# Kernel optimization log

Hardware: AMD Instinct MI355X
Metric: run time of the kernel (lower is better)

The kernel has to match this reference:

```python
import jax, jax.numpy as jnp
import numpy as np

B, N, H, D, HID = 4, 1024, 16, 72, 1152
ATT = H * D

def setup_inputs() -> dict:
    key = jax.random.key(0)
    ks = jax.random.split(key, 5)
    s = 0.02
    return {
        "x": jax.random.normal(ks[0], (B, N, HID), dtype=jnp.float32),
        "w_qkv": jax.random.normal(ks[1], (HID, 3 * ATT), dtype=jnp.float32) * s,
        "b_qkv": jnp.zeros((3 * ATT,), dtype=jnp.float32),
        "w_out": jax.random.normal(ks[2], (ATT, HID), dtype=jnp.float32) * s,
        "b_out": jnp.zeros((HID,), dtype=jnp.float32),
    }

def reference(x, w_qkv, b_qkv, w_out, b_out):
    # QKV projection: [B,N,3*ATT]
    qkv = x @ w_qkv + b_qkv
    q, k, v = jnp.split(qkv, 3, axis=-1)
    # [B,N,H,D] -> [B,H,N,D]
    q = q.reshape(B, N, H, D).transpose(0, 2, 1, 3)
    k = k.reshape(B, N, H, D).transpose(0, 2, 1, 3)
    v = v.reshape(B, N, H, D).transpose(0, 2, 1, 3)
    scale = D ** -0.5
    att = jnp.einsum("bhqd,bhkd->bhqk", q, k) * scale
    att = jax.nn.softmax(att, axis=-1)
    out = jnp.einsum("bhqk,bhkd->bhqd", att, v)
    out = out.transpose(0, 2, 1, 3).reshape(B, N, ATT)
    return out @ w_out + b_out
```

## Files before the change

kernel.cpp:

```cpp
#include <hip/hip_runtime.h>
#include <cstdint>

#define NB 4
#define NSEQ 1024
#define NH 16
#define HD 72
#define HID 1152
#define QKV3 3456
#define DP 96
#define QSCALE 0.17003713711193175f

typedef __attribute__((ext_vector_type(8))) __bf16 bf16x8;
typedef __attribute__((ext_vector_type(4))) __bf16 bf16x4;
typedef __attribute__((ext_vector_type(4))) float f32x4;

#define AS1 __attribute__((address_space(1)))
#define AS3 __attribute__((address_space(3)))

__device__ __forceinline__ void gl_lds16(const void* g, void* l) {
    __builtin_amdgcn_global_load_lds((const AS1 uint32_t*)g, (AS3 uint32_t*)l, 16, 0, 0);
}

#define RAW_BAR() asm volatile("s_barrier" ::: "memory")

__device__ __forceinline__ float fast_exp2(float x) {
    float r;
    asm("v_exp_f32 %0, %1" : "=v"(r) : "v"(x));
    return r;
}

#define XB_OFF     0UL
#define WQKVT_OFF  9437184UL
#define WOUTT_OFF  17694720UL
#define QP_OFF     20643840UL
#define KP_OFF     33226752UL
#define VT_OFF     45809664UL


__global__ void prep_kernel(const float* __restrict__ x, __bf16* __restrict__ xb,
                            const float* __restrict__ w_qkv, __bf16* __restrict__ wqkvT,
                            const float* __restrict__ w_out, __bf16* __restrict__ woutT,
                            __bf16* __restrict__ Qp, __bf16* __restrict__ Kp,
                            __bf16* __restrict__ Vt) {
    __shared__ float t[32][33];
    const int blk = blockIdx.x, tid = threadIdx.x;
    if (blk < 4608) {
        long i = (long)blk * 256 + tid;
        float4 v = ((const float4*)x)[i];
        bf16x4 o = { (__bf16)v.x, (__bf16)v.y, (__bf16)v.z, (__bf16)v.w };
        ((bf16x4*)xb)[i] = o;
    } else if (blk < 9792) {
        const float* in;  __bf16* outp;  int Nc, K, n0, k0;
        if (blk < 8496) {
            int b = blk - 4608; in = w_qkv; outp = wqkvT; Nc = QKV3; K = HID;
            n0 = (b % 108) * 32; k0 = (b / 108) * 32;
        } else {
            int b = blk - 8496; in = w_out; outp = woutT; Nc = HID; K = HID;
            n0 = (b % 36) * 32; k0 = (b / 36) * 32;
        }
        int xx = tid & 31, yy = tid >> 5;
        #pragma unroll
        for (int i = 0; i < 32; i += 8)
            t[yy + i][xx] = in[(long)(k0 + yy + i) * Nc + n0 + xx];
        __syncthreads();
        #pragma unroll
        for (int i = 0; i < 32; i += 8)
            outp[(long)(n0 + yy + i) * K + k0 + xx] = (__bf16)t[xx][yy + i];
    } else {
        int i = (blk - 9792) * 256 + tid;
        uint4 z = make_uint4(0u, 0u, 0u, 0u);
        if (i < 131072) {
            __bf16* base = (i & 65536) ? Kp : Qp;
            int row = i & 65535;
            uint4* p = (uint4*)(base + row * 96 + 72);
            p[0] = z; p[1] = z; p[2] = z;
        } else {
            int j = i - 131072;
            int bh = j / 1536, w = j - bh * 1536;
            *((uint4*)(Vt + (long)bh * 98304 + 73728) + w) = z;
        }
    }
}


template<int MT>
__device__ __forceinline__ void gemm_core(
    const __bf16* __restrict__ A, const __bf16* __restrict__ Bt,
    int lda, int ldb, int ntk, long rowA0, long rowB0,
    char* lds, f32x4 acc[MT][4])
{
    constexpr int BM    = MT * 32;
    constexpr int ATILE = BM * 64;
    constexpr int TILE  = ATILE + 256 * 64;
    constexpr int L     = BM / 128 + 2;

    const int tid  = threadIdx.x;
    const int wave = tid >> 6, lane = tid & 63;
    const int wm = wave >> 2, wn = wave & 3;
    const int lhi = lane >> 4, llo = lane & 15;
    const int srow = tid >> 2;
    const int scol = (tid & 3) * 8;

    auto stage = [&](int kt, int buf) {
        char* base = lds + buf * TILE;
        #pragma unroll
        for (int j = 0; j < BM / 128; ++j) {
            int r  = srow + j * 128;
            int ks = scol ^ ((((unsigned)r >> 1) & 3) << 3);
            gl_lds16(A + (rowA0 + r) * (long)lda + kt * 32 + ks, base + tid * 16 + j * 8192);
        }
        #pragma unroll
        for (int j = 0; j < 2; ++j) {
            int r  = srow + j * 128;
            int ks = scol ^ ((((unsigned)r >> 1) & 3) << 3);
            gl_lds16(Bt + (rowB0 + r) * (long)ldb + kt * 32 + ks,
                     base + ATILE + tid * 16 + j * 8192);
        }
    };

    stage(0, 0);
    stage(1, 1);
    asm volatile("s_waitcnt vmcnt(%0)" :: "n"(L) : "memory");
    RAW_BAR();

    int buf = 0;
    #pragma unroll 1
    for (int t = 0; t < ntk; ++t) {
        char* Ab = lds + buf * TILE;
        char* Bb = Ab + ATILE;
        int nb = buf + 2; if (nb >= 3) nb -= 3;
        if (t + 2 < ntk) stage(t + 2, nb);

        bf16x8 bfr[4];
        #pragma unroll
        for (int nt = 0; nt < 4; ++nt) {
            int R = wn * 64 + nt * 16 + llo;
            int b = (R * 64 + lhi * 16) ^ ((((unsigned)R >> 1) & 3) << 4);
            bfr[nt] = *(const bf16x8*)(Bb + b);
        }
        bf16x8 af[MT / 2];
        #pragma unroll
        for (int mt = 0; mt < MT / 2; ++mt) {
            int R = wm * (BM / 2) + mt * 16 + llo;
            int b = (R * 64 + lhi * 16) ^ ((((unsigned)R >> 1) & 3) << 4);
            af[mt] = *(const bf16x8*)(Ab + b);
        }
        __builtin_amdgcn_s_setprio(1);
        #pragma unroll
        for (int mt = 0; mt < MT / 2; ++mt)
            #pragma unroll
            for (int nt = 0; nt < 4; ++nt)
                acc[mt][nt] = __builtin_amdgcn_mfma_f32_16x16x32_bf16(af[mt], bfr[nt], acc[mt][nt], 0, 0, 0);
        __builtin_amdgcn_s_setprio(0);
        #pragma unroll
        for (int mt = 0; mt < MT / 2; ++mt) {
            int R = wm * (BM / 2) + (MT / 2 + mt) * 16 + llo;
            int b = (R * 64 + lhi * 16) ^ ((((unsigned)R >> 1) & 3) << 4);
            af[mt] = *(const bf16x8*)(Ab + b);
        }
        __builtin_amdgcn_s_setprio(1);
        #pragma unroll
        for (int mt = 0; mt < MT / 2; ++mt)
            #pragma unroll
            for (int nt = 0; nt < 4; ++nt)
                acc[MT / 2 + mt][nt] = __builtin_amdgcn_mfma_f32_16x16x32_bf16(af[mt], bfr[nt], acc[MT / 2 + mt][nt], 0, 0, 0);
        __builtin_amdgcn_s_setprio(0);
        if (t + 2 < ntk)      asm volatile("s_waitcnt vmcnt(%0)" :: "n"(L) : "memory");
        else if (t + 1 < ntk) asm volatile("s_waitcnt vmcnt(0)" ::: "memory");
        RAW_BAR();
        buf = (buf == 2) ? 0 : buf + 1;
    }
}


__global__ __launch_bounds__(512, 4) void gemm_qkv_kernel(
    const __bf16* __restrict__ xb, const __bf16* __restrict__ wqkvT,
    const float* __restrict__ b_qkv,
    __bf16* __restrict__ Qp, __bf16* __restrict__ Kp, __bf16* __restrict__ Vt)
{
    __shared__ char lds[73728];
    f32x4 acc[4][4];
    #pragma unroll
    for (int i = 0; i < 4; ++i)
        #pragma unroll
        for (int j = 0; j < 4; ++j) acc[i][j] = (f32x4){0.f, 0.f, 0.f, 0.f};

    int lin = blockIdx.x;
    int xcd = lin & 7, l = lin >> 3;
    int lbx = l / 7;
    int bx  = (xcd & 3) * 8 + lbx;
    int by  = (xcd >> 2) * 7 + (l - lbx * 7);
    long rowA0 = (long)bx * 128, rowB0 = (long)by * 256;

    gemm_core<4>(xb, wqkvT, HID, HID, HID / 32, rowA0, rowB0, lds, acc);

    const int wave = threadIdx.x >> 6, lane = threadIdx.x & 63;
    const int wm = wave >> 2, wn = wave & 3, lhi = lane >> 4, llo = lane & 15;

    #pragma unroll
    for (int nt = 0; nt < 4; ++nt) {
        int n = (int)rowB0 + wn * 64 + nt * 16 + llo;
        if (n >= QKV3) continue;
        int sec = n / HID;
        int nn  = n - sec * HID;
        int h   = nn / HD;
        int d   = nn - h * HD;
        float bias = b_qkv[n];
        if (sec == 2) {
            #pragma unroll
            for (int mt = 0; mt < 4; ++mt) {
                int m0 = (int)rowA0 + wm * 64 + mt * 16 + lhi * 4;
                int bb = m0 >> 10, nq0 = m0 & 1023;
                bf16x4 pk = { (__bf16)(acc[mt][nt][0] + bias), (__bf16)(acc[mt][nt][1] + bias),
                              (__bf16)(acc[mt][nt][2] + bias), (__bf16)(acc[mt][nt][3] + bias) };
                *(bf16x4*)(Vt + ((long)(bb * NH + h) * DP + d) * NSEQ + nq0) = pk;
            }
        } else {
            __bf16* dst = (sec == 0) ? Qp : Kp;
            float scl = (sec == 0) ? QSCALE : 1.0f;
            #pragma unroll
            for (int mt = 0; mt < 4; ++mt) {
                #pragma unroll
                for (int r = 0; r < 4; ++r) {
                    int m = (int)rowA0 + wm * 64 + mt * 16 + lhi * 4 + r;
                    int bb = m >> 10, nq = m & 1023;
                    long bhn = (long)(bb * NH + h) * NSEQ + nq;
                    dst[bhn * DP + d] = (__bf16)((acc[mt][nt][r] + bias) * scl);
                }
            }
        }
    }
}


__global__ __launch_bounds__(512, 4) void flash_kernel(
    const __bf16* __restrict__ Qp, const __bf16* __restrict__ Kp,
    const __bf16* __restrict__ Vt, __bf16* __restrict__ atto)
{
    __shared__ char lds[73728];
    const int tid  = threadIdx.x;
    const int wave = tid >> 6, lane = tid & 63;
    const int lhi = lane >> 4, llo = lane & 15;

    int lin = blockIdx.x;
    int v   = ((lin & 7) << 6) + (lin >> 3);
    const int qx = v & 7;
    const int bh = v >> 3;

    const __bf16* Qb  = Qp + (long)bh * NSEQ * DP;
    const char*   KbB = (const char*)(Kp + (long)bh * NSEQ * DP);
    const char*   VbB = (const char*)(Vt + (long)bh * DP * NSEQ);

    char* P = lds + 57344 + wave * 2048;
    const int q0 = qx * 128 + wave * 16;

    long soK[2]; int ldK[2];
    #pragma unroll
    for (int j = 0; j < 2; ++j) {
        int bk  = wave * 2 + j;
        int key = bk * 4 + (lane >> 4);
        int c   = (lane & 15) * 16;
        soK[j] = (long)key * 192 + (c ^ ((key & 15) << 4));
        ldK[j] = bk * 1024;
    }
    const int dv1 = wave * 8 + (lane >> 3);
    const int cV  = (lane & 7) * 16;
    const long soV1 = (long)dv1 * 2048 + (cV ^ ((dv1 & 7) << 4));
    const int dv2 = 64 + wave * 8 + (lane >> 3);
    const long soV2 = (long)dv2 * 2048 + (cV ^ ((dv2 & 7) << 4));
    const int ldV1 = wave * 1024, ldV2 = 8192 + wave * 1024;

    int kro[4][3], vro[2][5], pwo[4], pro[2];
    #pragma unroll
    for (int ct = 0; ct < 4; ++ct)
        #pragma unroll
        for (int dc = 0; dc < 3; ++dc)
            kro[ct][dc] = ((ct * 16 + llo) * 256 + dc * 64 + lhi * 16) ^ ((llo & 15) << 4);
    #pragma unroll
    for (int nc = 0; nc < 2; ++nc)
        #pragma unroll
        for (int t = 0; t < 5; ++t)
            vro[nc][t] = ((t * 16 + llo) * 128 + nc * 64 + lhi * 16) ^ ((llo & 7) << 4);
    #pragma unroll
    for (int ct = 0; ct < 4; ++ct)
        pwo[ct] = (llo * 128 + ct * 32 + lhi * 8) ^ ((llo & 7) << 4);
    #pragma unroll
    for (int nc = 0; nc < 2; ++nc)
        pro[nc] = (llo * 128 + nc * 64 + lhi * 16) ^ ((llo & 7) << 4);

    auto stageK = [&](int kt, int kbuf) {
        #pragma unroll
        for (int j = 0; j < 2; ++j)
            gl_lds16(KbB + kt * 12288 + soK[j], lds + kbuf * 16384 + ldK[j]);
    };
    auto stageV = [&](int kt, int vb) {
        gl_lds16(VbB + soV1 + kt * 128, lds + 32768 + vb * 12288 + ldV1);
        if (wave < 4)
            gl_lds16(VbB + soV2 + kt * 128, lds + 32768 + vb * 12288 + ldV2);
    };

    bf16x8 aq[3];
    #pragma unroll
    for (int dc = 0; dc < 3; ++dc)
        aq[dc] = *(const bf16x8*)(Qb + (long)(q0 + llo) * DP + dc * 32 + lhi * 8);

    float mr = -3.0e38f, lr = 0.f;
    f32x4 acc[5];
    #pragma unroll
    for (int t = 0; t < 5; ++t) acc[t] = (f32x4){0.f, 0.f, 0.f, 0.f};

    stageK(0, 0);
    stageV(0, 0);
    asm volatile("s_waitcnt vmcnt(0)" ::: "memory");
    RAW_BAR();

    #pragma unroll 2
    for (int kb = 0; kb < 16; ++kb) {
        const int buf = kb & 1;
        if (kb < 15) {
            stageK(kb + 1, buf ^ 1);
            stageV(kb + 1, buf ^ 1);
        }

        f32x4 s[4];
        __builtin_amdgcn_s_setprio(1);
        #pragma unroll
        for (int ct = 0; ct < 4; ++ct) {
            f32x4 z = (f32x4){0.f, 0.f, 0.f, 0.f};
            #pragma unroll
            for (int dc = 0; dc < 3; ++dc) {
                bf16x8 kf = *(const bf16x8*)(lds + buf * 16384 + kro[ct][dc]);
                z = __builtin_amdgcn_mfma_f32_16x16x32_bf16(kf, aq[dc], z, 0, 0, 0);
            }
            s[ct] = z;
        }
        __builtin_amdgcn_s_setprio(0);

        float m0 = fmaxf(fmaxf(s[0][0], s[0][1]), fmaxf(s[0][2], s[0][3]));
        float m1 = fmaxf(fmaxf(s[1][0], s[1][1]), fmaxf(s[1][2], s[1][3]));
        float m2 = fmaxf(fmaxf(s[2][0], s[2][1]), fmaxf(s[2][2], s[2][3]));
        float m3 = fmaxf(fmaxf(s[3][0], s[3][1]), fmaxf(s[3][2], s[3][3]));
        float mx = fmaxf(fmaxf(m0, m1), fmaxf(m2, m3));
        mx = fmaxf(mx, __shfl_xor(mx, 16, 64));
        mx = fmaxf(mx, __shfl_xor(mx, 32, 64));
        if (!__all(mx <= mr + 8.0f)) {
            float mn = fmaxf(mr, mx);
            float al = fast_exp2(mr - mn);
            mr = mn;
            lr *= al;
            #pragma unroll
            for (int t = 0; t < 5; ++t)
                #pragma unroll
                for (int r = 0; r < 4; ++r) acc[t][r] *= al;
        }
        float p[4][4]; float sm = 0.f;
        #pragma unroll
        for (int ct = 0; ct < 4; ++ct)
            #pragma unroll
            for (int r = 0; r < 4; ++r) { p[ct][r] = fast_exp2(s[ct][r] - mr); sm += p[ct][r]; }
        sm += __shfl_xor(sm, 16, 64);
        sm += __shfl_xor(sm, 32, 64);
        lr += sm;
        #pragma unroll
        for (int ct = 0; ct < 4; ++ct) {
            bf16x4 pk = { (__bf16)p[ct][0], (__bf16)p[ct][1], (__bf16)p[ct][2], (__bf16)p[ct][3] };
            *(bf16x4*)(P + pwo[ct]) = pk;
        }
        asm volatile("s_waitcnt lgkmcnt(0)" ::: "memory");

        __builtin_amdgcn_s_setprio(1);
        #pragma unroll
        for (int nc = 0; nc < 2; ++nc) {
            bf16x8 pP = *(const bf16x8*)(P + pro[nc]);
            #pragma unroll
            for (int t = 0; t < 5; ++t) {
                bf16x8 bv = *(const bf16x8*)(lds + 32768 + buf * 12288 + vro[nc][t]);
                acc[t] = __builtin_amdgcn_mfma_f32_16x16x32_bf16(bv, pP, acc[t], 0, 0, 0);
            }
        }
        __builtin_amdgcn_s_setprio(0);

        if (kb < 15) asm volatile("s_waitcnt vmcnt(0)" ::: "memory");
        RAW_BAR();
    }

    const float linv = 1.f / lr;
    const int b = bh >> 4, h = bh & 15;
    const int q = q0 + llo;
    __bf16* outP = atto + (long)(b * NSEQ + q) * HID + h * HD;
    #pragma unroll
    for (int t = 0; t < 5; ++t) {
        int d0 = t * 16 + lhi * 4;
        if (d0 < HD) {
            bf16x4 o = { (__bf16)(acc[t][0] * linv), (__bf16)(acc[t][1] * linv),
                         (__bf16)(acc[t][2] * linv), (__bf16)(acc[t][3] * linv) };
            *(bf16x4*)(outP + d0) = o;
        }
    }
}


__global__ __launch_bounds__(512, 4) void gemm_out_kernel(
    const __bf16* __restrict__ atto, const __bf16* __restrict__ woutT,
    const float* __restrict__ b_out, float* __restrict__ out)
{
    __shared__ char lds[73728];
    f32x4 acc[4][4];
    #pragma unroll
    for (int i = 0; i < 4; ++i)
        #pragma unroll
        for (int j = 0; j < 4; ++j) acc[i][j] = (f32x4){0.f, 0.f, 0.f, 0.f};

    int lin = blockIdx.x;
    int v   = (lin & 7) * 20 + (lin >> 3);
    int bx  = v / 5, by = v - bx * 5;
    long rowA0 = (long)bx * 128, rowB0 = (long)by * 256;

    gemm_core<4>(atto, woutT, HID, HID, HID / 32, rowA0, rowB0, lds, acc);

    const int wave = threadIdx.x >> 6, lane = threadIdx.x & 63;
    const int wm = wave >> 2, wn = wave & 3, lhi = lane >> 4, llo = lane & 15;

    #pragma unroll
    for (int nt = 0; nt < 4; ++nt) {
        int n = (int)rowB0 + wn * 64 + nt * 16 + llo;
        if (n >= HID) continue;
        float bias = b_out[n];
        #pragma unroll
        for (int mt = 0; mt < 4; ++mt) {
            #pragma unroll
            for (int r = 0; r < 4; ++r) {
                int m = (int)rowA0 + wm * 64 + mt * 16 + lhi * 4 + r;
                out[(long)m * HID + n] = acc[mt][nt][r] + bias;
            }
        }
    }
}


extern "C" void kernel_launch(void* const* d_in, const int* in_sizes, int n_in,
                              void* d_out, int out_size, void* d_ws, size_t ws_size,
                              hipStream_t stream) {
    const float* x      = (const float*)d_in[0];
    const float* w_qkv  = (const float*)d_in[1];
    const float* b_qkv  = (const float*)d_in[2];
    const float* w_out  = (const float*)d_in[3];
    const float* b_out  = (const float*)d_in[4];
    float* out = (float*)d_out;
    char* ws = (char*)d_ws;

    __bf16* xb    = (__bf16*)(ws + XB_OFF);
    __bf16* atto  = (__bf16*)(ws + XB_OFF);
    __bf16* wqkvT = (__bf16*)(ws + WQKVT_OFF);
    __bf16* woutT = (__bf16*)(ws + WOUTT_OFF);
    __bf16* Qp    = (__bf16*)(ws + QP_OFF);
    __bf16* Kp    = (__bf16*)(ws + KP_OFF);
    __bf16* Vt    = (__bf16*)(ws + VT_OFF);

    prep_kernel<<<10688, 256, 0, stream>>>(x, xb, w_qkv, wqkvT, w_out, woutT, Qp, Kp, Vt);
    gemm_qkv_kernel<<<448, 512, 0, stream>>>(xb, wqkvT, b_qkv, Qp, Kp, Vt);
    flash_kernel<<<512, 512, 0, stream>>>(Qp, Kp, Vt, atto);
    gemm_out_kernel<<<160, 512, 0, stream>>>(atto, woutT, b_out, out);
}
```

Baseline: 118.5 us.

## Load GEMM B operand directly into registers, stage only A through LDS

```diff
diff --git a/kernel.cpp b/kernel.cpp
--- a/kernel.cpp
+++ b/kernel.cpp
@@ -91,8 +91,6 @@
 {
     constexpr int BM    = MT * 32;
     constexpr int ATILE = BM * 64;
-    constexpr int TILE  = ATILE + 256 * 64;
-    constexpr int L     = BM / 128 + 2;
 
     const int tid  = threadIdx.x;
     const int wave = tid >> 6, lane = tid & 63;
@@ -101,71 +99,68 @@
     const int srow = tid >> 2;
     const int scol = (tid & 3) * 8;
 
-    auto stage = [&](int kt, int buf) {
-        char* base = lds + buf * TILE;
-        #pragma unroll
-        for (int j = 0; j < BM / 128; ++j) {
-            int r  = srow + j * 128;
-            int ks = scol ^ ((((unsigned)r >> 1) & 3) << 3);
-            gl_lds16(A + (rowA0 + r) * (long)lda + kt * 32 + ks, base + tid * 16 + j * 8192);
-        }
-        #pragma unroll
-        for (int j = 0; j < 2; ++j) {
-            int r  = srow + j * 128;
-            int ks = scol ^ ((((unsigned)r >> 1) & 3) << 3);
-            gl_lds16(Bt + (rowB0 + r) * (long)ldb + kt * 32 + ks,
-                     base + ATILE + tid * 16 + j * 8192);
-        }
-    };
-
-    stage(0, 0);
-    stage(1, 1);
-    asm volatile("s_waitcnt vmcnt(%0)" :: "n"(L) : "memory");
+    const int ksw = scol ^ ((((unsigned)srow >> 1) & 3) << 3);
+    const __bf16* aSrc = A + (rowA0 + srow) * (long)lda + ksw;
+    const int aDst = tid * 16;
+
+    int boffA[MT];
+    #pragma unroll
+    for (int mt = 0; mt < MT; ++mt) {
+        int R = wm * (BM / 2) + mt * 16 + llo;
+        boffA[mt] = (R * 64 + lhi * 16) ^ ((((unsigned)R >> 1) & 3) << 4);
+    }
+    const __bf16* bp[4];
+    #pragma unroll
+    for (int nt = 0; nt < 4; ++nt) {
+        int R = wn * 64 + nt * 16 + llo;
+        bp[nt] = Bt + (rowB0 + R) * (long)ldb + lhi * 8;
+    }
+
+    bf16x8 Bc[4];
+
+    gl_lds16(aSrc,      lds + aDst);
+    gl_lds16(aSrc + 32, lds + ATILE + aDst);
+    #pragma unroll
+    for (int nt = 0; nt < 4; ++nt) Bc[nt] = *(const bf16x8*)(bp[nt]);
+    asm volatile("s_waitcnt vmcnt(0)" ::: "memory");
     RAW_BAR();
 
     int buf = 0;
     #pragma unroll 1
     for (int t = 0; t < ntk; ++t) {
-        char* Ab = lds + buf * TILE;
-        char* Bb = Ab + ATILE;
+        char* Ab = lds + buf * ATILE;
         int nb = buf + 2; if (nb >= 3) nb -= 3;
-        if (t + 2 < ntk) stage(t + 2, nb);
-
-        bf16x8 bfr[4];
-        #pragma unroll
-        for (int nt = 0; nt < 4; ++nt) {
-            int R = wn * 64 + nt * 16 + llo;
-            int b = (R * 64 + lhi * 16) ^ ((((unsigned)R >> 1) & 3) << 4);
-            bfr[nt] = *(const bf16x8*)(Bb + b);
-        }
+
         bf16x8 af[MT / 2];
         #pragma unroll
-        for (int mt = 0; mt < MT / 2; ++mt) {
-            int R = wm * (BM / 2) + mt * 16 + llo;
-            int b = (R * 64 + lhi * 16) ^ ((((unsigned)R >> 1) & 3) << 4);
-            af[mt] = *(const bf16x8*)(Ab + b);
-        }
+        for (int mt = 0; mt < MT / 2; ++mt)
+            af[mt] = *(const bf16x8*)(Ab + boffA[mt]);
         __builtin_amdgcn_s_setprio(1);
         #pragma unroll
         for (int mt = 0; mt < MT / 2; ++mt)
             #pragma unroll
             for (int nt = 0; nt < 4; ++nt)
-                acc[mt][nt] = __builtin_amdgcn_mfma_f32_16x16x32_bf16(af[mt], bfr[nt], acc[mt][nt], 0, 0, 0);
+                acc[mt][nt] = __builtin_amdgcn_mfma_f32_16x16x32_bf16(af[mt], Bc[nt], acc[mt][nt], 0, 0, 0);
         __builtin_amdgcn_s_setprio(0);
         #pragma unroll
-        for (int mt = 0; mt < MT / 2; ++mt) {
-            int R = wm * (BM / 2) + (MT / 2 + mt) * 16 + llo;
-            int b = (R * 64 + lhi * 16) ^ ((((unsigned)R >> 1) & 3) << 4);
-            af[mt] = *(const bf16x8*)(Ab + b);
-        }
+        for (int mt = 0; mt < MT / 2; ++mt)
+            af[mt] = *(const bf16x8*)(Ab + boffA[MT / 2 + mt]);
         __builtin_amdgcn_s_setprio(1);
         #pragma unroll
         for (int mt = 0; mt < MT / 2; ++mt)
             #pragma unroll
             for (int nt = 0; nt < 4; ++nt)
-                acc[MT / 2 + mt][nt] = __builtin_amdgcn_mfma_f32_16x16x32_bf16(af[mt], bfr[nt], acc[MT / 2 + mt][nt], 0, 0, 0);
+                acc[MT / 2 + mt][nt] = __builtin_amdgcn_mfma_f32_16x16x32_bf16(af[mt], Bc[nt], acc[MT / 2 + mt][nt], 0, 0, 0);
         __builtin_amdgcn_s_setprio(0);
-        if (t + 2 < ntk)      asm volatile("s_waitcnt vmcnt(%0)" :: "n"(L) : "memory");
+
+        if (t + 1 < ntk) {
+            #pragma unroll
+            for (int nt = 0; nt < 4; ++nt)
+                Bc[nt] = *(const bf16x8*)(bp[nt] + (t + 1) * 32);
+        }
+        if (t + 2 < ntk) gl_lds16(aSrc + (t + 2) * 32, lds + nb * ATILE + aDst);
+
+        if (t + 2 < ntk)      asm volatile("s_waitcnt vmcnt(1)" ::: "memory");
         else if (t + 1 < ntk) asm volatile("s_waitcnt vmcnt(0)" ::: "memory");
         RAW_BAR();
         buf = (buf == 2) ? 0 : buf + 1;
@@ -173,12 +168,12 @@
 }
 
 
-__global__ __launch_bounds__(512, 4) void gemm_qkv_kernel(
+__global__ __launch_bounds__(512, 6) void gemm_qkv_kernel(
     const __bf16* __restrict__ xb, const __bf16* __restrict__ wqkvT,
     const float* __restrict__ b_qkv,
     __bf16* __restrict__ Qp, __bf16* __restrict__ Kp, __bf16* __restrict__ Vt)
 {
-    __shared__ char lds[73728];
+    __shared__ char lds[24576];
     f32x4 acc[4][4];
     #pragma unroll
     for (int i = 0; i < 4; ++i)
@@ -400,11 +395,11 @@
 }
 
 
-__global__ __launch_bounds__(512, 4) void gemm_out_kernel(
+__global__ __launch_bounds__(512, 6) void gemm_out_kernel(
     const __bf16* __restrict__ atto, const __bf16* __restrict__ woutT,
     const float* __restrict__ b_out, float* __restrict__ out)
 {
-    __shared__ char lds[73728];
+    __shared__ char lds[24576];
     f32x4 acc[4][4];
     #pragma unroll
     for (int i = 0; i < 4; ++i)
```

New measurement: 409.7 us. 246% more time.
